# Performance work log

Measured on AMD Instinct MI355X. Metric: run time of the kernel, lower is better.

The kernel has to match this reference:

```python
import jax, jax.numpy as jnp
import numpy as np

N_NODES = 50000


def _degree_norm(src, dst, n):
    # symmetric GCN normalization with self-loops already appended
    deg = jax.ops.segment_sum(jnp.ones(src.shape[0], jnp.float32), dst, num_segments=n)
    dinv = jnp.where(deg > 0, jax.lax.rsqrt(deg), 0.0)
    return dinv[src] * dinv[dst]  # [E_full]


def _gcn_layer(x, W, b, src, dst, norm, n):
    h = x @ W                                  # [N, out]
    msgs = h[src] * norm[:, None]              # gather + scale, [E_full, out]
    out = jax.ops.segment_sum(msgs, dst, num_segments=n)
    return out + b


def setup_inputs() -> dict:
    key = jax.random.key(0)
    k1, k2, k3, k4 = jax.random.split(key, 4)
    n, e, d_in, d_out = N_NODES, 800000, 256, 128
    x = jax.random.normal(k1, (n, d_in), jnp.float32)
    edge_index = jax.random.randint(k2, (2, e), 0, n, dtype=jnp.int64)
    W1 = jax.random.normal(k3, (d_in, 2 * d_out), jnp.float32) / np.sqrt(d_in)
    b1 = jnp.zeros((2 * d_out,), jnp.float32)
    W2 = jax.random.normal(k4, (2 * d_out, d_out), jnp.float32) / np.sqrt(2 * d_out)
    b2 = jnp.zeros((d_out,), jnp.float32)
    return {"x": x, "edge_index": edge_index, "W1": W1, "b1": b1, "W2": W2, "b2": b2}


def reference(x, edge_index, W1, b1, W2, b2):
    n = x.shape[0]
    loops = jnp.arange(n, dtype=edge_index.dtype)
    src = jnp.concatenate([edge_index[0], loops])
    dst = jnp.concatenate([edge_index[1], loops])
    norm = _degree_norm(src, dst, n)
    h = jax.nn.relu(_gcn_layer(x, W1, b1, src, dst, norm, n))
    h = jax.nn.relu(_gcn_layer(h, W2, b2, src, dst, norm, n))
    return h
```

## Files before the change

### kernel.cpp

```cpp
#include <hip/hip_runtime.h>
#include <hip/hip_bf16.h>


typedef __attribute__((ext_vector_type(8))) short bf16x8;
typedef __attribute__((ext_vector_type(4))) float f32x4;

__device__ inline float bf2f(unsigned short u) {
    return __uint_as_float(((unsigned)u) << 16);
}
__device__ inline unsigned short f2bf(float f) {
    unsigned x = __float_as_uint(f);
    unsigned r = (x + 0x7fffu + ((x >> 16) & 1u)) >> 16;
    return (unsigned short)r;
}

__global__ void degree_kernel(const int* __restrict__ dst, unsigned* __restrict__ deg, int E) {
    int e = blockIdx.x * blockDim.x + threadIdx.x;
    if (e < E) atomicAdd(&deg[dst[e]], 1u);
}

__global__ void dinv_kernel(const unsigned* __restrict__ deg, float* __restrict__ dinv, int N) {
    int i = blockIdx.x * blockDim.x + threadIdx.x;
    if (i < N) dinv[i] = rsqrtf((float)(deg[i] + 1u));
}

__global__ __launch_bounds__(1024) void scan_kernel(const unsigned* __restrict__ deg,
                                                    int* __restrict__ rowptr,
                                                    int* __restrict__ cursor, int N) {
    __shared__ int wsum[16];
    __shared__ int carry_s;
    const int t = threadIdx.x, lane = t & 63, w = t >> 6;
    if (t == 0) carry_s = 0;
    __syncthreads();
    for (int base = 0; base < N; base += 1024) {
        int i = base + t;
        int v = (i < N) ? (int)deg[i] : 0;
        int x = v;
#pragma unroll
        for (int off = 1; off < 64; off <<= 1) {
            int y = __shfl_up(x, off, 64);
            if (lane >= off) x += y;
        }
        if (lane == 63) wsum[w] = x;
        __syncthreads();
        if (w == 0 && lane < 16) {
            int s = wsum[lane];
#pragma unroll
            for (int off = 1; off < 16; off <<= 1) {
                int y = __shfl_up(s, off, 16);
                if ((lane & 15) >= off) s += y;
            }
            wsum[lane] = s;
        }
        __syncthreads();
        int waveoff = (w == 0) ? 0 : wsum[w - 1];
        int incl = x + waveoff;
        int excl = incl - v;
        int c = carry_s;
        if (i < N) { rowptr[i] = c + excl; cursor[i] = c + excl; }
        __syncthreads();
        if (t == 1023) carry_s = c + incl;
        __syncthreads();
    }
    if (t == 0) rowptr[N] = carry_s;
}

__global__ __launch_bounds__(256) void fill_kernel(const int* __restrict__ src,
                                                   const int* __restrict__ dst,
                                                   const float* __restrict__ dinv,
                                                   int* __restrict__ cursor,
                                                   int* __restrict__ col,
                                                   float* __restrict__ wgt, int E) {
    int e = blockIdx.x * blockDim.x + threadIdx.x;
    if (e < E) {
        int d = dst[e];
        int s = src[e];
        int pos = atomicAdd(&cursor[d], 1);
        col[pos] = s;
        wgt[pos] = dinv[s] * dinv[d];
    }
}

__global__ __launch_bounds__(256) void convert_x_kernel(const float* __restrict__ in,
                                                        unsigned short* __restrict__ out,
                                                        long n4) {
    long i = (long)blockIdx.x * blockDim.x + threadIdx.x;
    if (i < n4) {
        float4 v = ((const float4*)in)[i];
        ushort4 o;
        o.x = f2bf(v.x); o.y = f2bf(v.y); o.z = f2bf(v.z); o.w = f2bf(v.w);
        ((ushort4*)out)[i] = o;
    }
}

__global__ __launch_bounds__(256) void convert_wt_kernel(const float* __restrict__ W,
                                                         unsigned short* __restrict__ WT,
                                                         int K, int Nw) {
    int id = blockIdx.x * blockDim.x + threadIdx.x;
    if (id < K * Nw) {
        int k = id / Nw;
        int n = id % Nw;
        WT[(long)n * K + k] = f2bf(W[id]);
    }
}

#define GBM 128
#define GBN 128
#define GBK 64
__global__ __launch_bounds__(256) void gemm_bf16(const unsigned short* __restrict__ A,
                                                 const unsigned short* __restrict__ BT,
                                                 unsigned short* __restrict__ C,
                                                 int M, int Nc, int K) {
    __shared__ __align__(16) unsigned short As[GBM * GBK];
    __shared__ __align__(16) unsigned short Bs[GBN * GBK];
    const int t = threadIdx.x;
    const int lane = t & 63;
    const int w = t >> 6;
    const int row0 = blockIdx.x * GBM;
    const int col0 = blockIdx.y * GBN;
    const int rb = (w >> 1) * 64;
    const int cb = (w & 1) * 64;

    f32x4 acc[4][4] = {};

    for (int kb = 0; kb < K; kb += GBK) {
#pragma unroll
        for (int i = 0; i < 4; i++) {
            int p = i * 256 + t;
            int row = p >> 3;
            int slot = p & 7;
            int chunk = slot ^ (row & 7);
            int grow = row0 + row;
            if (grow >= M) grow = M - 1;
            const unsigned short* src = A + (size_t)grow * K + kb + chunk * 8;
            __builtin_amdgcn_global_load_lds(
                (const __attribute__((address_space(1))) void*)src,
                (__attribute__((address_space(3))) void*)&As[p * 8], 16, 0, 0);
        }
#pragma unroll
        for (int i = 0; i < 4; i++) {
            int p = i * 256 + t;
            int row = p >> 3;
            int slot = p & 7;
            int chunk = slot ^ (row & 7);
            const unsigned short* src = BT + (size_t)(col0 + row) * K + kb + chunk * 8;
            __builtin_amdgcn_global_load_lds(
                (const __attribute__((address_space(1))) void*)src,
                (__attribute__((address_space(3))) void*)&Bs[p * 8], 16, 0, 0);
        }
        asm volatile("s_waitcnt vmcnt(0)" ::: "memory");
        __syncthreads();

#pragma unroll
        for (int ks = 0; ks < 2; ks++) {
            int kq = ks * 4 + (lane >> 4);
            int rsel = lane & 15;
            bf16x8 af[4], bfr[4];
#pragma unroll
            for (int mt = 0; mt < 4; mt++) {
                int m = rb + mt * 16 + rsel;
                int slot = kq ^ (m & 7);
                af[mt] = *(const bf16x8*)&As[m * GBK + slot * 8];
            }
#pragma unroll
            for (int nt = 0; nt < 4; nt++) {
                int n = cb + nt * 16 + rsel;
                int slot = kq ^ (n & 7);
                bfr[nt] = *(const bf16x8*)&Bs[n * GBK + slot * 8];
            }
#pragma unroll
            for (int mt = 0; mt < 4; mt++)
#pragma unroll
                for (int nt = 0; nt < 4; nt++)
                    acc[mt][nt] = __builtin_amdgcn_mfma_f32_16x16x32_bf16(
                        af[mt], bfr[nt], acc[mt][nt], 0, 0, 0);
        }
        __syncthreads();
    }

#pragma unroll
    for (int mt = 0; mt < 4; mt++) {
#pragma unroll
        for (int nt = 0; nt < 4; nt++) {
            int gcol = col0 + cb + nt * 16 + (lane & 15);
            int grow0 = row0 + rb + mt * 16 + 4 * (lane >> 4);
#pragma unroll
            for (int r = 0; r < 4; r++) {
                int g = grow0 + r;
                if (g < M) C[(size_t)g * Nc + gcol] = f2bf(acc[mt][nt][r]);
            }
        }
    }
}

template <bool OUT_BF16>
__global__ void gather_kernel(const unsigned short* __restrict__ h,
                              const int* __restrict__ rowptr,
                              const int* __restrict__ col,
                              const float* __restrict__ wgt,
                              const float* __restrict__ dinv,
                              const float* __restrict__ bias,
                              void* __restrict__ out,
                              int F) {
    const int node = blockIdx.x;
    const int f0 = 2 * threadIdx.x;
    const int beg = rowptr[node];
    const int end = rowptr[node + 1];

    float a0 = 0.f, a1 = 0.f;
    int e = beg;
    for (; e + 4 <= end; e += 4) {
        int s0 = col[e], s1 = col[e + 1], s2 = col[e + 2], s3 = col[e + 3];
        float w0 = wgt[e], w1 = wgt[e + 1], w2 = wgt[e + 2], w3 = wgt[e + 3];
        ushort2 u0 = *(const ushort2*)&h[(size_t)s0 * F + f0];
        ushort2 u1 = *(const ushort2*)&h[(size_t)s1 * F + f0];
        ushort2 u2 = *(const ushort2*)&h[(size_t)s2 * F + f0];
        ushort2 u3 = *(const ushort2*)&h[(size_t)s3 * F + f0];
        a0 += bf2f(u0.x) * w0 + bf2f(u1.x) * w1 + bf2f(u2.x) * w2 + bf2f(u3.x) * w3;
        a1 += bf2f(u0.y) * w0 + bf2f(u1.y) * w1 + bf2f(u2.y) * w2 + bf2f(u3.y) * w3;
    }
    for (; e < end; e++) {
        int s = col[e];
        float wv = wgt[e];
        ushort2 u = *(const ushort2*)&h[(size_t)s * F + f0];
        a0 += bf2f(u.x) * wv;
        a1 += bf2f(u.y) * wv;
    }
    float di = dinv[node];
    ushort2 us = *(const ushort2*)&h[(size_t)node * F + f0];
    float2 bv = *(const float2*)&bias[f0];
    float v0 = fmaxf(a0 + bf2f(us.x) * di * di + bv.x, 0.f);
    float v1 = fmaxf(a1 + bf2f(us.y) * di * di + bv.y, 0.f);
    if (OUT_BF16) {
        ushort2 o; o.x = f2bf(v0); o.y = f2bf(v1);
        *(ushort2*)&((unsigned short*)out)[(size_t)node * F + f0] = o;
    } else {
        float2 o; o.x = v0; o.y = v1;
        *(float2*)&((float*)out)[(size_t)node * F + f0] = o;
    }
}

extern "C" void kernel_launch(void* const* d_in, const int* in_sizes, int n_in,
                              void* d_out, int out_size, void* d_ws, size_t ws_size,
                              hipStream_t stream) {
    const float* x  = (const float*)d_in[0];
    const int* ei   = (const int*)d_in[1];
    const float* W1 = (const float*)d_in[2];
    const float* b1 = (const float*)d_in[3];
    const float* W2 = (const float*)d_in[4];
    const float* b2 = (const float*)d_in[5];

    const int DIN = 256;
    const int N = in_sizes[0] / DIN;
    const int E = in_sizes[1] / 2;
    const int H = in_sizes[3];
    const int DOUT = in_sizes[5];

    const int* src = ei;
    const int* dst = ei + E;

    char* ws = (char*)d_ws;
    unsigned* deg = (unsigned*)ws;                   ws += (size_t)N * 4;
    float* dinv   = (float*)ws;                      ws += (size_t)N * 4;
    int* rowptr   = (int*)ws;                        ws += (size_t)(N + 4) * 4;
    int* cursor   = (int*)ws;                        ws += (size_t)N * 4;
    int* col      = (int*)ws;                        ws += (size_t)E * 4;
    float* wgt    = (float*)ws;                      ws += (size_t)E * 4;
    unsigned short* xb  = (unsigned short*)ws;       ws += (size_t)N * DIN * 2;
    unsigned short* w1t = (unsigned short*)ws;       ws += (size_t)DIN * H * 2;
    unsigned short* w2t = (unsigned short*)ws;       ws += (size_t)H * DOUT * 2;
    unsigned short* h1b = (unsigned short*)ws;       ws += (size_t)N * H * 2;
    unsigned short* y1b = (unsigned short*)ws;       ws += (size_t)N * H * 2;
    unsigned short* h2b = xb;
    float* outp = (float*)d_out;

    hipMemsetAsync(deg, 0, (size_t)N * 4, stream);
    degree_kernel<<<(E + 255) / 256, 256, 0, stream>>>(dst, deg, E);
    dinv_kernel<<<(N + 255) / 256, 256, 0, stream>>>(deg, dinv, N);
    scan_kernel<<<1, 1024, 0, stream>>>(deg, rowptr, cursor, N);
    fill_kernel<<<(E + 255) / 256, 256, 0, stream>>>(src, dst, dinv, cursor, col, wgt, E);

    {
        long n4 = (long)N * DIN / 4;
        convert_x_kernel<<<(int)((n4 + 255) / 256), 256, 0, stream>>>(x, xb, n4);
        convert_wt_kernel<<<(DIN * H + 255) / 256, 256, 0, stream>>>(W1, w1t, DIN, H);
        convert_wt_kernel<<<(H * DOUT + 255) / 256, 256, 0, stream>>>(W2, w2t, H, DOUT);
    }

    {
        dim3 grid((N + GBM - 1) / GBM, H / GBN);
        gemm_bf16<<<grid, 256, 0, stream>>>(xb, w1t, h1b, N, H, DIN);
    }
    gather_kernel<true><<<N, H / 2, 0, stream>>>(h1b, rowptr, col, wgt, dinv, b1, y1b, H);

    {
        dim3 grid((N + GBM - 1) / GBM, DOUT / GBN);
        gemm_bf16<<<grid, 256, 0, stream>>>(y1b, w2t, h2b, N, DOUT, H);
    }
    gather_kernel<false><<<N, DOUT / 2, 0, stream>>>(h2b, rowptr, col, wgt, dinv, b2, outp, DOUT);
}
```

Before: 380.1 us.

## Chunk GEMM outputs feature-major, gather per-chunk with waves, parallelize scan

```diff
diff --git a/kernel.cpp b/kernel.cpp
--- a/kernel.cpp
+++ b/kernel.cpp
@@ -24,16 +24,54 @@
     if (i < N) dinv[i] = rsqrtf((float)(deg[i] + 1u));
 }
 
-__global__ __launch_bounds__(1024) void scan_kernel(const unsigned* __restrict__ deg,
-                                                    int* __restrict__ rowptr,
-                                                    int* __restrict__ cursor, int N) {
-    __shared__ int wsum[16];
-    __shared__ int carry_s;
+#define SCAN_CHUNK 2048
+
+__global__ __launch_bounds__(256) void scan_phase1(const unsigned* __restrict__ deg,
+                                                   int* __restrict__ bsum, int N) {
+    __shared__ int ws[4];
     const int t = threadIdx.x, lane = t & 63, w = t >> 6;
-    if (t == 0) carry_s = 0;
+    int base = blockIdx.x * SCAN_CHUNK;
+    int s = 0;
+#pragma unroll
+    for (int r = 0; r < SCAN_CHUNK / 256; r++) {
+        int i = base + r * 256 + t;
+        s += (i < N) ? (int)deg[i] : 0;
+    }
+#pragma unroll
+    for (int off = 1; off < 64; off <<= 1) s += __shfl_xor(s, off, 64);
+    if (lane == 0) ws[w] = s;
     __syncthreads();
-    for (int base = 0; base < N; base += 1024) {
-        int i = base + t;
+    if (t == 0) bsum[blockIdx.x] = ws[0] + ws[1] + ws[2] + ws[3];
+}
+
+__global__ void scan_phase2(int* __restrict__ bsum, int nb) {
+    const int t = threadIdx.x;
+    int carry = 0;
+    for (int b = 0; b < nb; b += 64) {
+        int i = b + t;
+        int v = (i < nb) ? bsum[i] : 0;
+        int x = v;
+#pragma unroll
+        for (int off = 1; off < 64; off <<= 1) {
+            int y = __shfl_up(x, off, 64);
+            if (t >= off) x += y;
+        }
+        if (i < nb) bsum[i] = carry + x - v;
+        carry += __shfl(x, 63, 64);
+    }
+}
+
+__global__ __launch_bounds__(256) void scan_phase3(const unsigned* __restrict__ deg,
+                                                   const int* __restrict__ bsum,
+                                                   int* __restrict__ rowptr,
+                                                   int* __restrict__ cursor, int N) {
+    __shared__ int ws[4];
+    const int t = threadIdx.x, lane = t & 63, w = t >> 6;
+    int base = blockIdx.x * SCAN_CHUNK;
+    int carry = bsum[blockIdx.x];
+#pragma unroll
+    for (int r = 0; r < SCAN_CHUNK / 256; r++) {
+        int i = base + r * 256 + t;
         int v = (i < N) ? (int)deg[i] : 0;
         int x = v;
 #pragma unroll
@@ -41,43 +79,28 @@
             int y = __shfl_up(x, off, 64);
             if (lane >= off) x += y;
         }
-        if (lane == 63) wsum[w] = x;
+        if (lane == 63) ws[w] = x;
         __syncthreads();
-        if (w == 0 && lane < 16) {
-            int s = wsum[lane];
-#pragma unroll
-            for (int off = 1; off < 16; off <<= 1) {
-                int y = __shfl_up(s, off, 16);
-                if ((lane & 15) >= off) s += y;
-            }
-            wsum[lane] = s;
-        }
+        int wo = 0;
+        for (int j = 0; j < w; j++) wo += ws[j];
+        int excl = x + wo - v;
+        if (i < N) { rowptr[i] = carry + excl; cursor[i] = carry + excl; }
+        int total = ws[0] + ws[1] + ws[2] + ws[3];
         __syncthreads();
-        int waveoff = (w == 0) ? 0 : wsum[w - 1];
-        int incl = x + waveoff;
-        int excl = incl - v;
-        int c = carry_s;
-        if (i < N) { rowptr[i] = c + excl; cursor[i] = c + excl; }
-        __syncthreads();
-        if (t == 1023) carry_s = c + incl;
-        __syncthreads();
-    }
-    if (t == 0) rowptr[N] = carry_s;
+        carry += total;
+    }
+    if (blockIdx.x == gridDim.x - 1 && t == 0) rowptr[N] = carry;
 }
 
 __global__ __launch_bounds__(256) void fill_kernel(const int* __restrict__ src,
                                                    const int* __restrict__ dst,
-                                                   const float* __restrict__ dinv,
                                                    int* __restrict__ cursor,
-                                                   int* __restrict__ col,
-                                                   float* __restrict__ wgt, int E) {
+                                                   int* __restrict__ col, int E) {
     int e = blockIdx.x * blockDim.x + threadIdx.x;
     if (e < E) {
         int d = dst[e];
-        int s = src[e];
         int pos = atomicAdd(&cursor[d], 1);
-        col[pos] = s;
-        wgt[pos] = dinv[s] * dinv[d];
+        col[pos] = src[e];
     }
 }
 
@@ -107,6 +130,7 @@
 #define GBM 128
 #define GBN 128
 #define GBK 64
+template <int CH>
 __global__ __launch_bounds__(256) void gemm_bf16(const unsigned short* __restrict__ A,
                                                  const unsigned short* __restrict__ BT,
                                                  unsigned short* __restrict__ C,
@@ -183,60 +207,82 @@
 #pragma unroll
         for (int nt = 0; nt < 4; nt++) {
             int gcol = col0 + cb + nt * 16 + (lane & 15);
+            int c = gcol / CH;
+            int fo = gcol % CH;
             int grow0 = row0 + rb + mt * 16 + 4 * (lane >> 4);
 #pragma unroll
             for (int r = 0; r < 4; r++) {
                 int g = grow0 + r;
-                if (g < M) C[(size_t)g * Nc + gcol] = f2bf(acc[mt][nt][r]);
+                if (g < M)
+                    C[((size_t)c * M + g) * CH + fo] = f2bf(acc[mt][nt][r]);
             }
         }
     }
 }
 
-template <bool OUT_BF16>
-__global__ void gather_kernel(const unsigned short* __restrict__ h,
-                              const int* __restrict__ rowptr,
-                              const int* __restrict__ col,
-                              const float* __restrict__ wgt,
-                              const float* __restrict__ dinv,
-                              const float* __restrict__ bias,
-                              void* __restrict__ out,
-                              int F) {
-    const int node = blockIdx.x;
-    const int f0 = 2 * threadIdx.x;
+template <int CH, bool OUT_BF16>
+__global__ __launch_bounds__(256) void gather_cm_kernel(
+    const unsigned short* __restrict__ h_cm,
+    const int* __restrict__ rowptr,
+    const int* __restrict__ col,
+    const float* __restrict__ dinv,
+    const float* __restrict__ bias,
+    void* __restrict__ out,
+    int Nn, int F) {
+    const int bid = blockIdx.x;
+    const int chunk = bid & 7;
+    const int nb = bid >> 3;
+    const int wv = threadIdx.x >> 6;
+    const int lane = threadIdx.x & 63;
+    const int node = nb * 4 + wv;
+    if (node >= Nn) return;
+
+    constexpr int LF = CH / 2;
+    constexpr int NE = 64 / LF;
+    const int fl = lane & (LF - 1);
+    const int eg = lane / LF;
+
+    const unsigned short* hc = h_cm + (size_t)chunk * Nn * CH;
     const int beg = rowptr[node];
     const int end = rowptr[node + 1];
+    const float ddst = dinv[node];
 
     float a0 = 0.f, a1 = 0.f;
-    int e = beg;
-    for (; e + 4 <= end; e += 4) {
-        int s0 = col[e], s1 = col[e + 1], s2 = col[e + 2], s3 = col[e + 3];
-        float w0 = wgt[e], w1 = wgt[e + 1], w2 = wgt[e + 2], w3 = wgt[e + 3];
-        ushort2 u0 = *(const ushort2*)&h[(size_t)s0 * F + f0];
-        ushort2 u1 = *(const ushort2*)&h[(size_t)s1 * F + f0];
-        ushort2 u2 = *(const ushort2*)&h[(size_t)s2 * F + f0];
-        ushort2 u3 = *(const ushort2*)&h[(size_t)s3 * F + f0];
-        a0 += bf2f(u0.x) * w0 + bf2f(u1.x) * w1 + bf2f(u2.x) * w2 + bf2f(u3.x) * w3;
-        a1 += bf2f(u0.y) * w0 + bf2f(u1.y) * w1 + bf2f(u2.y) * w2 + bf2f(u3.y) * w3;
-    }
-    for (; e < end; e++) {
+    int e = beg + eg;
+    for (; e + NE < end; e += 2 * NE) {
+        int s0 = col[e], s1 = col[e + NE];
+        float w0 = dinv[s0] * ddst;
+        float w1 = dinv[s1] * ddst;
+        ushort2 u0 = *(const ushort2*)&hc[(size_t)s0 * CH + 2 * fl];
+        ushort2 u1 = *(const ushort2*)&hc[(size_t)s1 * CH + 2 * fl];
+        a0 += bf2f(u0.x) * w0 + bf2f(u1.x) * w1;
+        a1 += bf2f(u0.y) * w0 + bf2f(u1.y) * w1;
+    }
+    if (e < end) {
         int s = col[e];
-        float wv = wgt[e];
-        ushort2 u = *(const ushort2*)&h[(size_t)s * F + f0];
-        a0 += bf2f(u.x) * wv;
-        a1 += bf2f(u.y) * wv;
-    }
-    float di = dinv[node];
-    ushort2 us = *(const ushort2*)&h[(size_t)node * F + f0];
-    float2 bv = *(const float2*)&bias[f0];
-    float v0 = fmaxf(a0 + bf2f(us.x) * di * di + bv.x, 0.f);
-    float v1 = fmaxf(a1 + bf2f(us.y) * di * di + bv.y, 0.f);
-    if (OUT_BF16) {
-        ushort2 o; o.x = f2bf(v0); o.y = f2bf(v1);
-        *(ushort2*)&((unsigned short*)out)[(size_t)node * F + f0] = o;
-    } else {
-        float2 o; o.x = v0; o.y = v1;
-        *(float2*)&((float*)out)[(size_t)node * F + f0] = o;
+        float wv2 = dinv[s] * ddst;
+        ushort2 u = *(const ushort2*)&hc[(size_t)s * CH + 2 * fl];
+        a0 += bf2f(u.x) * wv2;
+        a1 += bf2f(u.y) * wv2;
+    }
+#pragma unroll
+    for (int off = LF; off < 64; off <<= 1) {
+        a0 += __shfl_xor(a0, off, 64);
+        a1 += __shfl_xor(a1, off, 64);
+    }
+    if (lane < LF) {
+        int f0 = chunk * CH + 2 * fl;
+        ushort2 us = *(const ushort2*)&hc[(size_t)node * CH + 2 * fl];
+        float2 bv = *(const float2*)&bias[f0];
+        float v0 = fmaxf(a0 + bf2f(us.x) * ddst * ddst + bv.x, 0.f);
+        float v1 = fmaxf(a1 + bf2f(us.y) * ddst * ddst + bv.y, 0.f);
+        if (OUT_BF16) {
+            ushort2 o; o.x = f2bf(v0); o.y = f2bf(v1);
+            *(ushort2*)&((unsigned short*)out)[(size_t)node * F + f0] = o;
+        } else {
+            float2 o; o.x = v0; o.y = v1;
+            *(float2*)&((float*)out)[(size_t)node * F + f0] = o;
+        }
     }
 }
 
@@ -263,9 +309,9 @@
     unsigned* deg = (unsigned*)ws;                   ws += (size_t)N * 4;
     float* dinv   = (float*)ws;                      ws += (size_t)N * 4;
     int* rowptr   = (int*)ws;                        ws += (size_t)(N + 4) * 4;
+    int* bsum     = (int*)ws;                        ws += 64 * 4;
     int* cursor   = (int*)ws;                        ws += (size_t)N * 4;
     int* col      = (int*)ws;                        ws += (size_t)E * 4;
-    float* wgt    = (float*)ws;                      ws += (size_t)E * 4;
     unsigned short* xb  = (unsigned short*)ws;       ws += (size_t)N * DIN * 2;
     unsigned short* w1t = (unsigned short*)ws;       ws += (size_t)DIN * H * 2;
     unsigned short* w2t = (unsigned short*)ws;       ws += (size_t)H * DOUT * 2;
@@ -277,8 +323,13 @@
     hipMemsetAsync(deg, 0, (size_t)N * 4, stream);
     degree_kernel<<<(E + 255) / 256, 256, 0, stream>>>(dst, deg, E);
     dinv_kernel<<<(N + 255) / 256, 256, 0, stream>>>(deg, dinv, N);
-    scan_kernel<<<1, 1024, 0, stream>>>(deg, rowptr, cursor, N);
-    fill_kernel<<<(E + 255) / 256, 256, 0, stream>>>(src, dst, dinv, cursor, col, wgt, E);
+    {
+        int nb = (N + SCAN_CHUNK - 1) / SCAN_CHUNK;
+        scan_phase1<<<nb, 256, 0, stream>>>(deg, bsum, N);
+        scan_phase2<<<1, 64, 0, stream>>>(bsum, nb);
+        scan_phase3<<<nb, 256, 0, stream>>>(deg, bsum, rowptr, cursor, N);
+    }
+    fill_kernel<<<(E + 255) / 256, 256, 0, stream>>>(src, dst, cursor, col, E);
 
     {
         long n4 = (long)N * DIN / 4;
@@ -289,13 +340,15 @@
 
     {
         dim3 grid((N + GBM - 1) / GBM, H / GBN);
-        gemm_bf16<<<grid, 256, 0, stream>>>(xb, w1t, h1b, N, H, DIN);
-    }
-    gather_kernel<true><<<N, H / 2, 0, stream>>>(h1b, rowptr, col, wgt, dinv, b1, y1b, H);
+        gemm_bf16<32><<<grid, 256, 0, stream>>>(xb, w1t, h1b, N, H, DIN);
+    }
+    gather_cm_kernel<32, true><<<8 * ((N + 3) / 4), 256, 0, stream>>>(
+        h1b, rowptr, col, dinv, b1, y1b, N, H);
 
     {
         dim3 grid((N + GBM - 1) / GBM, DOUT / GBN);
-        gemm_bf16<<<grid, 256, 0, stream>>>(y1b, w2t, h2b, N, DOUT, H);
-    }
-    gather_kernel<false><<<N, DOUT / 2, 0, stream>>>(h2b, rowptr, col, wgt, dinv, b2, outp, DOUT);
-}
+        gemm_bf16<16><<<grid, 256, 0, stream>>>(y1b, w2t, h2b, N, DOUT, H);
+    }
+    gather_cm_kernel<16, false><<<8 * ((N + 3) / 4), 256, 0, stream>>>(
+        h2b, rowptr, col, dinv, b2, outp, N, DOUT);
+}
```

Result: slower. 511.4 us (+34.5%).
